# Kernel optimization log

Measured on AMD Instinct MI355X. Metric: run time of the kernel, lower is better.

Reference implementation:

```python
import jax, jax.numpy as jnp
import numpy as np

D_MODEL = 1024
N_HEADS = 16
D_HEAD = 64
N_CTX = 2048
ROTARY_DIM = 64
ROTARY_BASE = 10000.0
ATTN_SCALE = 8.0
IGNORE = -100000.0


def _sin_cos(seq_len):
    # rotary_adjacent_pairs=False -> freq repeated as '(2 d)'
    pos = jnp.arange(seq_len, dtype=jnp.float32)
    dim = jnp.arange(ROTARY_DIM // 2, dtype=jnp.float32)
    freq = ROTARY_BASE ** (dim / (ROTARY_DIM / 2))
    freq = jnp.concatenate([freq, freq])  # (2 d)
    angles = pos[:, None] / freq[None, :]  # [S, rotary_dim]
    return jnp.sin(angles), jnp.cos(angles)


def _apply_rotary(x, sin, cos):
    # x: [B, S, H, d_head]; rotary_dim == d_head here, pass-through part is empty
    x_rot = x[..., :ROTARY_DIM]
    x_pass = x[..., ROTARY_DIM:]
    n = ROTARY_DIM // 2
    x_flip = jnp.concatenate([-x_rot[..., n:], x_rot[..., :n]], axis=-1)
    x_rotated = x_rot * cos[None, :, None, :] + x_flip * sin[None, :, None, :]
    return jnp.concatenate([x_rotated, x_pass], axis=-1)


def setup_inputs() -> dict:
    key = jax.random.key(0)
    ks = jax.random.split(key, 12)
    B, S = 1, 2048
    f = lambda k, shp, s=1.0: jax.random.normal(k, shp, dtype=jnp.float32) * s
    return {
        "xq": f(ks[0], (B, S, N_HEADS, D_MODEL)),
        "xk": f(ks[1], (B, S, N_HEADS, D_MODEL)),
        "xv": f(ks[2], (B, S, N_HEADS, D_MODEL)),
        "W_Q": f(ks[3], (N_HEADS, D_MODEL, D_HEAD), 0.02),
        "b_Q": jnp.zeros((N_HEADS, D_HEAD), jnp.float32),
        "W_K": f(ks[4], (N_HEADS, D_MODEL, D_HEAD), 0.02),
        "b_K": jnp.zeros((N_HEADS, D_HEAD), jnp.float32),
        "W_V": f(ks[5], (N_HEADS, D_MODEL, D_HEAD), 0.02),
        "b_V": jnp.zeros((N_HEADS, D_HEAD), jnp.float32),
        "W_O": f(ks[6], (N_HEADS, D_HEAD, D_MODEL), 0.02),
        "b_O": jnp.zeros((D_MODEL,), jnp.float32),
    }


def reference(xq, xk, xv, W_Q, b_Q, W_K, b_K, W_V, b_V, W_O, b_O):
    S = xq.shape[1]
    sin, cos = _sin_cos(S)
    # per-head QKV projections: [B,S,H,dm] x [H,dm,dh] -> [B,S,H,dh]
    q = jnp.einsum('bsnd,nde->bsne', xq, W_Q) + b_Q
    k = jnp.einsum('bsnd,nde->bsne', xk, W_K) + b_K
    v = jnp.einsum('bsnd,nde->bsne', xv, W_V) + b_V
    q = _apply_rotary(q, sin, cos)
    k = _apply_rotary(k, sin, cos)
    # attention scores [B,H,Q,K]
    scores = jnp.einsum('bqne,bkne->bnqk', q, k) / ATTN_SCALE
    causal = jnp.triu(jnp.ones((S, S), dtype=bool), k=1)
    scores = jnp.where(causal[None, None], IGNORE, scores)
    pattern = jax.nn.softmax(scores, axis=-1)
    z = jnp.einsum('bnqk,bkne->bqne', pattern, v)
    # NOTE: faithful to source — head dim is NOT summed; b_O divided by n_heads
    attn_out = jnp.einsum('bqne,ned->bqnd', z, W_O) + b_O / N_HEADS
    return attn_out
```

## Files before the change

### kernel.cpp

```cpp
#include <hip/hip_runtime.h>
#include <hip/hip_bf16.h>
#include <stdint.h>
#include <math.h>

typedef __bf16 bf16_t;
typedef __bf16 bf16x8 __attribute__((ext_vector_type(8)));
typedef __bf16 bf16x4 __attribute__((ext_vector_type(4)));
typedef float  f32x4  __attribute__((ext_vector_type(4)));

#define S_CTX 2048
#define NH    16
#define DM    1024
#define DH    64

#define WS_WT   0
#define WS_WOT  (3*1048576)
#define WS_Q    (4*1048576)
#define WS_K    (WS_Q  + 2097152)
#define WS_VT   (WS_K  + 2097152)
#define WS_Z    (WS_VT + 2097152)

__device__ __forceinline__ void stage_tile(const bf16_t* __restrict__ g, int row_stride,
                                           bf16_t* lds, int tid) {
#pragma unroll
  for (int i = 0; i < 2; i++) {
    int r = (tid >> 3) + i * 32;
    int c = (tid & 7) << 3;
    *reinterpret_cast<uint4*>(lds + r * 64 + c) =
        *reinterpret_cast<const uint4*>(g + r * row_stride + c);
  }
}

__device__ __forceinline__ void stage_f32(const float* __restrict__ g, int row_stride,
                                          bf16_t* lds, int tid) {
#pragma unroll
  for (int i = 0; i < 4; i++) {
    int idx = tid + i * 256;
    int r = idx >> 4;
    int c = (idx & 15) << 2;
    float4 v = *reinterpret_cast<const float4*>(g + r * row_stride + c);
    bf16x4 b;
    b[0] = (bf16_t)v.x; b[1] = (bf16_t)v.y; b[2] = (bf16_t)v.z; b[3] = (bf16_t)v.w;
    *reinterpret_cast<bf16x4*>(lds + r * 64 + c) = b;
  }
}

__global__ __launch_bounds__(256) void transpose_w(const float* __restrict__ wq,
                                                   const float* __restrict__ wk,
                                                   const float* __restrict__ wv,
                                                   const float* __restrict__ wo,
                                                   bf16_t* __restrict__ ws) {
  __shared__ bf16_t tl[64 * 68];
  int m = blockIdx.z, h = blockIdx.y, t = blockIdx.x, tid = threadIdx.x;
  const float* in; bf16_t* out; int R, C, r0, c0;
  if (m < 3) { in = (m == 0) ? wq : (m == 1) ? wk : wv; out = ws + m * 1048576;
               R = 1024; C = 64; r0 = t * 64; c0 = 0; }
  else       { in = wo; out = ws + WS_WOT; R = 64; C = 1024; r0 = 0; c0 = t * 64; }
  in  += h * 65536;
  out += h * 65536;
#pragma unroll
  for (int i = 0; i < 4; i++) {
    int idx = tid + i * 256;
    int r = idx >> 4, c = (idx & 15) << 2;
    float4 v = *reinterpret_cast<const float4*>(in + (r0 + r) * C + c0 + c);
    bf16x4 b;
    b[0] = (bf16_t)v.x; b[1] = (bf16_t)v.y; b[2] = (bf16_t)v.z; b[3] = (bf16_t)v.w;
    *reinterpret_cast<bf16x4*>(tl + r * 68 + c) = b;
  }
  __syncthreads();
#pragma unroll
  for (int i = 0; i < 2; i++) {
    int oc = (tid >> 3) + i * 32, ok = (tid & 7) << 3;
    bf16x8 v;
#pragma unroll
    for (int j = 0; j < 8; j++) v[j] = tl[(ok + j) * 68 + oc];
    *reinterpret_cast<bf16x8*>(out + (c0 + oc) * R + r0 + ok) = v;
  }
}

__global__ __launch_bounds__(256) void qkv_proj(const float* __restrict__ xq,
                                                const float* __restrict__ xk,
                                                const float* __restrict__ xv,
                                                const float* __restrict__ bq,
                                                const float* __restrict__ bk,
                                                const float* __restrict__ bv,
                                                bf16_t* __restrict__ ws) {
  __shared__ bf16_t Al[64 * 64];
  __shared__ bf16_t Bl[64 * 64];
  int st = blockIdx.x, h = blockIdx.y, m = blockIdx.z;
  int tid = threadIdx.x, w = tid >> 6, lane = tid & 63, quad = lane >> 4, l15 = lane & 15;
  const float*  in   = (m == 0) ? xq : (m == 1) ? xk : xv;
  const bf16_t* wT   = ws + m * 1048576 + h * 65536;
  const float*  bias = (m == 0) ? bq : (m == 1) ? bk : bv;
  int s0 = st * 64;
  f32x4 acc[4];
#pragma unroll
  for (int t = 0; t < 4; t++) acc[t] = (f32x4){0.f, 0.f, 0.f, 0.f};
  const float* Ab = in + (s0 * 16 + h) * 1024;

  for (int k0 = 0; k0 < 1024; k0 += 64) {
    stage_f32(Ab + k0, 16384, Al, tid);
    stage_tile(wT + k0, 1024, Bl, tid);
    __syncthreads();
#pragma unroll
    for (int ks = 0; ks < 2; ks++) {
      bf16x8 af = *reinterpret_cast<const bf16x8*>(Al + (w * 16 + l15) * 64 + ks * 32 + quad * 8);
#pragma unroll
      for (int t = 0; t < 4; t++) {
        bf16x8 bfr = *reinterpret_cast<const bf16x8*>(Bl + (t * 16 + l15) * 64 + ks * 32 + quad * 8);
        acc[t] = __builtin_amdgcn_mfma_f32_16x16x32_bf16(af, bfr, acc[t], 0, 0, 0);
      }
    }
    __syncthreads();
  }
#pragma unroll
  for (int t = 0; t < 4; t++) {
    float bval = bias[h * 64 + t * 16 + l15];
#pragma unroll
    for (int r = 0; r < 4; r++) acc[t][r] += bval;
  }

  if (m < 2) {
    bf16_t* outp = ws + ((m == 0) ? WS_Q : WS_K) + h * (2048 * 64);
#pragma unroll
    for (int t = 0; t < 2; t++) {
      int c_lo = t * 16 + l15;
      float freq = powf(10000.0f, (float)c_lo * (1.0f / 32.0f));
#pragma unroll
      for (int r = 0; r < 4; r++) {
        int s = s0 + w * 16 + quad * 4 + r;
        float ang = (float)s / freq;
        float sv = sinf(ang), cv = cosf(ang);
        float xl = acc[t][r], xh = acc[t + 2][r];
        acc[t][r]     = xl * cv - xh * sv;
        acc[t + 2][r] = xh * cv + xl * sv;
      }
    }
#pragma unroll
    for (int t = 0; t < 4; t++)
#pragma unroll
      for (int r = 0; r < 4; r++) {
        int s = s0 + w * 16 + quad * 4 + r;
        outp[s * 64 + t * 16 + l15] = (bf16_t)acc[t][r];
      }
  } else {
    bf16_t* outp = ws + WS_VT + h * (64 * 2048);
#pragma unroll
    for (int t = 0; t < 4; t++) {
      int e = t * 16 + l15;
      int s = s0 + w * 16 + quad * 4;
      bf16x4 v;
#pragma unroll
      for (int r = 0; r < 4; r++) v[r] = (bf16_t)acc[t][r];
      *reinterpret_cast<bf16x4*>(outp + e * 2048 + s) = v;
    }
  }
}

__global__ __launch_bounds__(256) void attn(bf16_t* __restrict__ ws) {
  __shared__ bf16_t Ql[64 * 64], Kl[64 * 64], Vl[64 * 64], Pl[4 * 16 * 64];
  int qt = blockIdx.x, h = blockIdx.y;
  int tid = threadIdx.x, w = tid >> 6, lane = tid & 63, quad = lane >> 4, l15 = lane & 15;
  const bf16_t* qp  = ws + WS_Q  + h * 131072;
  const bf16_t* kp  = ws + WS_K  + h * 131072;
  const bf16_t* vtp = ws + WS_VT + h * 131072;
  bf16_t*       zp  = ws + WS_Z  + h * 131072;
  int s0 = qt * 64;

  stage_tile(qp + s0 * 64, 64, Ql, tid);

  f32x4 o[4];
#pragma unroll
  for (int t = 0; t < 4; t++) o[t] = (f32x4){0.f, 0.f, 0.f, 0.f};
  float m_i[4], l_i[4];
#pragma unroll
  for (int r = 0; r < 4; r++) { m_i[r] = -__builtin_inff(); l_i[r] = 0.f; }

  for (int j = 0; j <= qt; j++) {
    __syncthreads();
    stage_tile(kp + j * 64 * 64, 64,   Kl, tid);
    stage_tile(vtp + j * 64,     2048, Vl, tid);
    __syncthreads();

    f32x4 sc[4];
#pragma unroll
    for (int t = 0; t < 4; t++) sc[t] = (f32x4){0.f, 0.f, 0.f, 0.f};
#pragma unroll
    for (int ks = 0; ks < 2; ks++) {
      bf16x8 af = *reinterpret_cast<const bf16x8*>(Ql + (w * 16 + l15) * 64 + ks * 32 + quad * 8);
#pragma unroll
      for (int t = 0; t < 4; t++) {
        bf16x8 bfr = *reinterpret_cast<const bf16x8*>(Kl + (t * 16 + l15) * 64 + ks * 32 + quad * 8);
        sc[t] = __builtin_amdgcn_mfma_f32_16x16x32_bf16(af, bfr, sc[t], 0, 0, 0);
      }
    }
#pragma unroll
    for (int t = 0; t < 4; t++) {
      int kvc = j * 64 + t * 16 + l15;
#pragma unroll
      for (int r = 0; r < 4; r++) {
        int qrow = s0 + w * 16 + quad * 4 + r;
        float sv = sc[t][r] * 0.125f;
        sc[t][r] = (kvc > qrow) ? -1e30f : sv;
      }
    }
    float p[4][4], alpha[4];
#pragma unroll
    for (int r = 0; r < 4; r++) {
      float mx = fmaxf(fmaxf(sc[0][r], sc[1][r]), fmaxf(sc[2][r], sc[3][r]));
#pragma unroll
      for (int off = 1; off < 16; off <<= 1) mx = fmaxf(mx, __shfl_xor(mx, off));
      float mn = fmaxf(m_i[r], mx);
      alpha[r] = __expf(m_i[r] - mn);
      float rs = 0.f;
#pragma unroll
      for (int t = 0; t < 4; t++) { p[t][r] = __expf(sc[t][r] - mn); rs += p[t][r]; }
#pragma unroll
      for (int off = 1; off < 16; off <<= 1) rs += __shfl_xor(rs, off);
      l_i[r] = l_i[r] * alpha[r] + rs;
      m_i[r] = mn;
    }
#pragma unroll
    for (int t = 0; t < 4; t++)
#pragma unroll
      for (int r = 0; r < 4; r++)
        Pl[w * 1024 + (quad * 4 + r) * 64 + t * 16 + l15] = (bf16_t)p[t][r];
#pragma unroll
    for (int t = 0; t < 4; t++)
#pragma unroll
      for (int r = 0; r < 4; r++) o[t][r] *= alpha[r];
    __syncthreads();
#pragma unroll
    for (int ks = 0; ks < 2; ks++) {
      bf16x8 af = *reinterpret_cast<const bf16x8*>(Pl + w * 1024 + l15 * 64 + ks * 32 + quad * 8);
#pragma unroll
      for (int t = 0; t < 4; t++) {
        bf16x8 bfr = *reinterpret_cast<const bf16x8*>(Vl + (t * 16 + l15) * 64 + ks * 32 + quad * 8);
        o[t] = __builtin_amdgcn_mfma_f32_16x16x32_bf16(af, bfr, o[t], 0, 0, 0);
      }
    }
  }
  float inv[4];
#pragma unroll
  for (int r = 0; r < 4; r++) inv[r] = 1.0f / l_i[r];
#pragma unroll
  for (int t = 0; t < 4; t++)
#pragma unroll
    for (int r = 0; r < 4; r++) {
      int s = s0 + w * 16 + quad * 4 + r;
      zp[s * 64 + t * 16 + l15] = (bf16_t)(o[t][r] * inv[r]);
    }
}

__global__ __launch_bounds__(256) void out_proj(const bf16_t* __restrict__ ws,
                                                const float* __restrict__ bo,
                                                float* __restrict__ out) {
  __shared__ bf16_t Al[64 * 64], Bl[64 * 64];
  int st = blockIdx.x >> 4, dt = blockIdx.x & 15, h = blockIdx.y;
  int tid = threadIdx.x, w = tid >> 6, lane = tid & 63, quad = lane >> 4, l15 = lane & 15;
  int s0 = st * 64, d0 = dt * 64;
  const bf16_t* zp = ws + WS_Z + h * 131072 + s0 * 64;
  const bf16_t* wo = ws + WS_WOT + h * 65536 + d0 * 64;
  stage_tile(zp, 64, Al, tid);
  stage_tile(wo, 64, Bl, tid);
  __syncthreads();
  f32x4 acc[4];
#pragma unroll
  for (int t = 0; t < 4; t++) acc[t] = (f32x4){0.f, 0.f, 0.f, 0.f};
#pragma unroll
  for (int ks = 0; ks < 2; ks++) {
    bf16x8 af = *reinterpret_cast<const bf16x8*>(Al + (w * 16 + l15) * 64 + ks * 32 + quad * 8);
#pragma unroll
    for (int t = 0; t < 4; t++) {
      bf16x8 bfr = *reinterpret_cast<const bf16x8*>(Bl + (t * 16 + l15) * 64 + ks * 32 + quad * 8);
      acc[t] = __builtin_amdgcn_mfma_f32_16x16x32_bf16(af, bfr, acc[t], 0, 0, 0);
    }
  }
#pragma unroll
  for (int t = 0; t < 4; t++) {
    float bval = bo[d0 + t * 16 + l15] * (1.0f / 16.0f);
#pragma unroll
    for (int r = 0; r < 4; r++) {
      int s = s0 + w * 16 + quad * 4 + r;
      out[(s * 16 + h) * 1024 + d0 + t * 16 + l15] = acc[t][r] + bval;
    }
  }
}

extern "C" void kernel_launch(void* const* d_in, const int* in_sizes, int n_in,
                              void* d_out, int out_size, void* d_ws, size_t ws_size,
                              hipStream_t stream) {
  const float* xq = (const float*)d_in[0];
  const float* xk = (const float*)d_in[1];
  const float* xv = (const float*)d_in[2];
  const float* wq = (const float*)d_in[3];
  const float* bq = (const float*)d_in[4];
  const float* wk = (const float*)d_in[5];
  const float* bk = (const float*)d_in[6];
  const float* wv = (const float*)d_in[7];
  const float* bv = (const float*)d_in[8];
  const float* wo = (const float*)d_in[9];
  const float* bo = (const float*)d_in[10];
  bf16_t* ws  = (bf16_t*)d_ws;
  float*  out = (float*)d_out;

  hipLaunchKernelGGL(transpose_w, dim3(16, 16, 4), dim3(256), 0, stream, wq, wk, wv, wo, ws);
  hipLaunchKernelGGL(qkv_proj,    dim3(32, 16, 3), dim3(256), 0, stream, xq, xk, xv, bq, bk, bv, ws);
  hipLaunchKernelGGL(attn,        dim3(32, 16),    dim3(256), 0, stream, ws);
  hipLaunchKernelGGL(out_proj,    dim3(512, 16),   dim3(256), 0, stream, ws, bo, out);
}
```

Baseline: 570.7 us.

## Enlarge tiles in projection and attention kernels and pad LDS rows

The QKV projection now computes 128 rows per block with a K step of 128, so each B fragment feeds two MFMAs and each block issues more global loads per barrier. The attention kernel processes 128-key tiles per iteration, halving the loop trip count. It also drops the block barrier before the P·V product, since each wave only reads its own P slice. The output projection uses 128x128 tiles, and all LDS tiles get padded row strides (72/136) to reduce bank conflicts. The cost is more LDS and registers per block, fewer blocks in flight, and some fully masked key columns on the last attention tile.

Result: faster. 556.6 us (-2.5%).

```diff
diff --git a/kernel.cpp b/kernel.cpp
--- a/kernel.cpp
+++ b/kernel.cpp
@@ -19,31 +19,6 @@
 #define WS_K    (WS_Q  + 2097152)
 #define WS_VT   (WS_K  + 2097152)
 #define WS_Z    (WS_VT + 2097152)
-
-__device__ __forceinline__ void stage_tile(const bf16_t* __restrict__ g, int row_stride,
-                                           bf16_t* lds, int tid) {
-#pragma unroll
-  for (int i = 0; i < 2; i++) {
-    int r = (tid >> 3) + i * 32;
-    int c = (tid & 7) << 3;
-    *reinterpret_cast<uint4*>(lds + r * 64 + c) =
-        *reinterpret_cast<const uint4*>(g + r * row_stride + c);
-  }
-}
-
-__device__ __forceinline__ void stage_f32(const float* __restrict__ g, int row_stride,
-                                          bf16_t* lds, int tid) {
-#pragma unroll
-  for (int i = 0; i < 4; i++) {
-    int idx = tid + i * 256;
-    int r = idx >> 4;
-    int c = (idx & 15) << 2;
-    float4 v = *reinterpret_cast<const float4*>(g + r * row_stride + c);
-    bf16x4 b;
-    b[0] = (bf16_t)v.x; b[1] = (bf16_t)v.y; b[2] = (bf16_t)v.z; b[3] = (bf16_t)v.w;
-    *reinterpret_cast<bf16x4*>(lds + r * 64 + c) = b;
-  }
-}
 
 __global__ __launch_bounds__(256) void transpose_w(const float* __restrict__ wq,
                                                    const float* __restrict__ wk,
@@ -85,30 +60,52 @@
                                                 const float* __restrict__ bk,
                                                 const float* __restrict__ bv,
                                                 bf16_t* __restrict__ ws) {
-  __shared__ bf16_t Al[64 * 64];
-  __shared__ bf16_t Bl[64 * 64];
+  __shared__ bf16_t Al[128 * 136];
+  __shared__ bf16_t Bl[64 * 136];
   int st = blockIdx.x, h = blockIdx.y, m = blockIdx.z;
   int tid = threadIdx.x, w = tid >> 6, lane = tid & 63, quad = lane >> 4, l15 = lane & 15;
   const float*  in   = (m == 0) ? xq : (m == 1) ? xk : xv;
   const bf16_t* wT   = ws + m * 1048576 + h * 65536;
   const float*  bias = (m == 0) ? bq : (m == 1) ? bk : bv;
-  int s0 = st * 64;
-  f32x4 acc[4];
-#pragma unroll
-  for (int t = 0; t < 4; t++) acc[t] = (f32x4){0.f, 0.f, 0.f, 0.f};
+  int s0 = st * 128;
   const float* Ab = in + (s0 * 16 + h) * 1024;
 
-  for (int k0 = 0; k0 < 1024; k0 += 64) {
-    stage_f32(Ab + k0, 16384, Al, tid);
-    stage_tile(wT + k0, 1024, Bl, tid);
+  f32x4 acc[2][4];
+#pragma unroll
+  for (int rt = 0; rt < 2; rt++)
+#pragma unroll
+    for (int t = 0; t < 4; t++) acc[rt][t] = (f32x4){0.f, 0.f, 0.f, 0.f};
+
+  for (int k0 = 0; k0 < 1024; k0 += 128) {
+#pragma unroll
+    for (int i = 0; i < 8; i++) {
+      int g = tid + i * 256;
+      int r = g >> 4, cg = g & 15;
+      const float* p = Ab + r * 16384 + k0 + cg * 8;
+      float4 v0 = *reinterpret_cast<const float4*>(p);
+      float4 v1 = *reinterpret_cast<const float4*>(p + 4);
+      bf16x8 b;
+      b[0] = (bf16_t)v0.x; b[1] = (bf16_t)v0.y; b[2] = (bf16_t)v0.z; b[3] = (bf16_t)v0.w;
+      b[4] = (bf16_t)v1.x; b[5] = (bf16_t)v1.y; b[6] = (bf16_t)v1.z; b[7] = (bf16_t)v1.w;
+      *reinterpret_cast<bf16x8*>(Al + r * 136 + cg * 8) = b;
+    }
+#pragma unroll
+    for (int i = 0; i < 4; i++) {
+      int g = tid + i * 256;
+      int r = g >> 4, cg = g & 15;
+      *reinterpret_cast<uint4*>(Bl + r * 136 + cg * 8) =
+          *reinterpret_cast<const uint4*>(wT + r * 1024 + k0 + cg * 8);
+    }
     __syncthreads();
 #pragma unroll
-    for (int ks = 0; ks < 2; ks++) {
-      bf16x8 af = *reinterpret_cast<const bf16x8*>(Al + (w * 16 + l15) * 64 + ks * 32 + quad * 8);
+    for (int ks = 0; ks < 4; ks++) {
+      bf16x8 a0 = *reinterpret_cast<const bf16x8*>(Al + (w * 32 + l15) * 136 + ks * 32 + quad * 8);
+      bf16x8 a1 = *reinterpret_cast<const bf16x8*>(Al + (w * 32 + 16 + l15) * 136 + ks * 32 + quad * 8);
 #pragma unroll
       for (int t = 0; t < 4; t++) {
-        bf16x8 bfr = *reinterpret_cast<const bf16x8*>(Bl + (t * 16 + l15) * 64 + ks * 32 + quad * 8);
-        acc[t] = __builtin_amdgcn_mfma_f32_16x16x32_bf16(af, bfr, acc[t], 0, 0, 0);
+        bf16x8 bb = *reinterpret_cast<const bf16x8*>(Bl + (t * 16 + l15) * 136 + ks * 32 + quad * 8);
+        acc[0][t] = __builtin_amdgcn_mfma_f32_16x16x32_bf16(a0, bb, acc[0][t], 0, 0, 0);
+        acc[1][t] = __builtin_amdgcn_mfma_f32_16x16x32_bf16(a1, bb, acc[1][t], 0, 0, 0);
       }
     }
     __syncthreads();
@@ -117,7 +114,9 @@
   for (int t = 0; t < 4; t++) {
     float bval = bias[h * 64 + t * 16 + l15];
 #pragma unroll
-    for (int r = 0; r < 4; r++) acc[t][r] += bval;
+    for (int rt = 0; rt < 2; rt++)
+#pragma unroll
+      for (int r = 0; r < 4; r++) acc[rt][t][r] += bval;
   }
 
   if (m < 2) {
@@ -127,38 +126,47 @@
       int c_lo = t * 16 + l15;
       float freq = powf(10000.0f, (float)c_lo * (1.0f / 32.0f));
 #pragma unroll
-      for (int r = 0; r < 4; r++) {
-        int s = s0 + w * 16 + quad * 4 + r;
-        float ang = (float)s / freq;
-        float sv = sinf(ang), cv = cosf(ang);
-        float xl = acc[t][r], xh = acc[t + 2][r];
-        acc[t][r]     = xl * cv - xh * sv;
-        acc[t + 2][r] = xh * cv + xl * sv;
-      }
-    }
-#pragma unroll
-    for (int t = 0; t < 4; t++)
-#pragma unroll
-      for (int r = 0; r < 4; r++) {
-        int s = s0 + w * 16 + quad * 4 + r;
-        outp[s * 64 + t * 16 + l15] = (bf16_t)acc[t][r];
-      }
+      for (int rt = 0; rt < 2; rt++)
+#pragma unroll
+        for (int r = 0; r < 4; r++) {
+          int s = s0 + w * 32 + rt * 16 + quad * 4 + r;
+          float ang = (float)s / freq;
+          float sv = sinf(ang), cv = cosf(ang);
+          float xl = acc[rt][t][r], xh = acc[rt][t + 2][r];
+          acc[rt][t][r]     = xl * cv - xh * sv;
+          acc[rt][t + 2][r] = xh * cv + xl * sv;
+        }
+    }
+#pragma unroll
+    for (int rt = 0; rt < 2; rt++)
+#pragma unroll
+      for (int t = 0; t < 4; t++)
+#pragma unroll
+        for (int r = 0; r < 4; r++) {
+          int s = s0 + w * 32 + rt * 16 + quad * 4 + r;
+          outp[s * 64 + t * 16 + l15] = (bf16_t)acc[rt][t][r];
+        }
   } else {
     bf16_t* outp = ws + WS_VT + h * (64 * 2048);
 #pragma unroll
-    for (int t = 0; t < 4; t++) {
-      int e = t * 16 + l15;
-      int s = s0 + w * 16 + quad * 4;
-      bf16x4 v;
-#pragma unroll
-      for (int r = 0; r < 4; r++) v[r] = (bf16_t)acc[t][r];
-      *reinterpret_cast<bf16x4*>(outp + e * 2048 + s) = v;
-    }
+    for (int rt = 0; rt < 2; rt++)
+#pragma unroll
+      for (int t = 0; t < 4; t++) {
+        int e = t * 16 + l15;
+        int sbase = s0 + w * 32 + rt * 16 + quad * 4;
+        bf16x4 v;
+#pragma unroll
+        for (int r = 0; r < 4; r++) v[r] = (bf16_t)acc[rt][t][r];
+        *reinterpret_cast<bf16x4*>(outp + e * 2048 + sbase) = v;
+      }
   }
 }
 
 __global__ __launch_bounds__(256) void attn(bf16_t* __restrict__ ws) {
-  __shared__ bf16_t Ql[64 * 64], Kl[64 * 64], Vl[64 * 64], Pl[4 * 16 * 64];
+  __shared__ bf16_t Ql[64 * 72];
+  __shared__ bf16_t Kl[128 * 72];
+  __shared__ bf16_t Vl[64 * 136];
+  __shared__ bf16_t Pl[4 * 16 * 136];
   int qt = blockIdx.x, h = blockIdx.y;
   int tid = threadIdx.x, w = tid >> 6, lane = tid & 63, quad = lane >> 4, l15 = lane & 15;
   const bf16_t* qp  = ws + WS_Q  + h * 131072;
@@ -167,7 +175,13 @@
   bf16_t*       zp  = ws + WS_Z  + h * 131072;
   int s0 = qt * 64;
 
-  stage_tile(qp + s0 * 64, 64, Ql, tid);
+#pragma unroll
+  for (int i = 0; i < 2; i++) {
+    int g = tid + i * 256;
+    int r = g >> 3, cg = g & 7;
+    *reinterpret_cast<uint4*>(Ql + r * 72 + cg * 8) =
+        *reinterpret_cast<const uint4*>(qp + (s0 + r) * 64 + cg * 8);
+  }
 
   f32x4 o[4];
 #pragma unroll
@@ -175,28 +189,42 @@
   float m_i[4], l_i[4];
 #pragma unroll
   for (int r = 0; r < 4; r++) { m_i[r] = -__builtin_inff(); l_i[r] = 0.f; }
-
-  for (int j = 0; j <= qt; j++) {
+  bf16_t* Plw = Pl + w * (16 * 136);
+
+  int jmax = qt >> 1;
+  for (int j = 0; j <= jmax; j++) {
     __syncthreads();
-    stage_tile(kp + j * 64 * 64, 64,   Kl, tid);
-    stage_tile(vtp + j * 64,     2048, Vl, tid);
+#pragma unroll
+    for (int i = 0; i < 4; i++) {
+      int g = tid + i * 256;
+      int r = g >> 3, cg = g & 7;
+      *reinterpret_cast<uint4*>(Kl + r * 72 + cg * 8) =
+          *reinterpret_cast<const uint4*>(kp + (j * 128 + r) * 64 + cg * 8);
+    }
+#pragma unroll
+    for (int i = 0; i < 4; i++) {
+      int g = tid + i * 256;
+      int r = g >> 4, cg = g & 15;
+      *reinterpret_cast<uint4*>(Vl + r * 136 + cg * 8) =
+          *reinterpret_cast<const uint4*>(vtp + r * 2048 + j * 128 + cg * 8);
+    }
     __syncthreads();
 
-    f32x4 sc[4];
-#pragma unroll
-    for (int t = 0; t < 4; t++) sc[t] = (f32x4){0.f, 0.f, 0.f, 0.f};
+    f32x4 sc[8];
+#pragma unroll
+    for (int t = 0; t < 8; t++) sc[t] = (f32x4){0.f, 0.f, 0.f, 0.f};
 #pragma unroll
     for (int ks = 0; ks < 2; ks++) {
-      bf16x8 af = *reinterpret_cast<const bf16x8*>(Ql + (w * 16 + l15) * 64 + ks * 32 + quad * 8);
-#pragma unroll
-      for (int t = 0; t < 4; t++) {
-        bf16x8 bfr = *reinterpret_cast<const bf16x8*>(Kl + (t * 16 + l15) * 64 + ks * 32 + quad * 8);
+      bf16x8 af = *reinterpret_cast<const bf16x8*>(Ql + (w * 16 + l15) * 72 + ks * 32 + quad * 8);
+#pragma unroll
+      for (int t = 0; t < 8; t++) {
+        bf16x8 bfr = *reinterpret_cast<const bf16x8*>(Kl + (t * 16 + l15) * 72 + ks * 32 + quad * 8);
         sc[t] = __builtin_amdgcn_mfma_f32_16x16x32_bf16(af, bfr, sc[t], 0, 0, 0);
       }
     }
 #pragma unroll
-    for (int t = 0; t < 4; t++) {
-      int kvc = j * 64 + t * 16 + l15;
+    for (int t = 0; t < 8; t++) {
+      int kvc = j * 128 + t * 16 + l15;
 #pragma unroll
       for (int r = 0; r < 4; r++) {
         int qrow = s0 + w * 16 + quad * 4 + r;
@@ -204,38 +232,39 @@
         sc[t][r] = (kvc > qrow) ? -1e30f : sv;
       }
     }
-    float p[4][4], alpha[4];
+    float alpha[4];
 #pragma unroll
     for (int r = 0; r < 4; r++) {
-      float mx = fmaxf(fmaxf(sc[0][r], sc[1][r]), fmaxf(sc[2][r], sc[3][r]));
+      float mx = sc[0][r];
+#pragma unroll
+      for (int t = 1; t < 8; t++) mx = fmaxf(mx, sc[t][r]);
 #pragma unroll
       for (int off = 1; off < 16; off <<= 1) mx = fmaxf(mx, __shfl_xor(mx, off));
       float mn = fmaxf(m_i[r], mx);
       alpha[r] = __expf(m_i[r] - mn);
       float rs = 0.f;
 #pragma unroll
-      for (int t = 0; t < 4; t++) { p[t][r] = __expf(sc[t][r] - mn); rs += p[t][r]; }
+      for (int t = 0; t < 8; t++) { sc[t][r] = __expf(sc[t][r] - mn); rs += sc[t][r]; }
 #pragma unroll
       for (int off = 1; off < 16; off <<= 1) rs += __shfl_xor(rs, off);
       l_i[r] = l_i[r] * alpha[r] + rs;
       m_i[r] = mn;
     }
 #pragma unroll
+    for (int t = 0; t < 8; t++)
+#pragma unroll
+      for (int r = 0; r < 4; r++)
+        Plw[(quad * 4 + r) * 136 + t * 16 + l15] = (bf16_t)sc[t][r];
+#pragma unroll
     for (int t = 0; t < 4; t++)
 #pragma unroll
-      for (int r = 0; r < 4; r++)
-        Pl[w * 1024 + (quad * 4 + r) * 64 + t * 16 + l15] = (bf16_t)p[t][r];
-#pragma unroll
-    for (int t = 0; t < 4; t++)
-#pragma unroll
       for (int r = 0; r < 4; r++) o[t][r] *= alpha[r];
-    __syncthreads();
-#pragma unroll
-    for (int ks = 0; ks < 2; ks++) {
-      bf16x8 af = *reinterpret_cast<const bf16x8*>(Pl + w * 1024 + l15 * 64 + ks * 32 + quad * 8);
+#pragma unroll
+    for (int ks = 0; ks < 4; ks++) {
+      bf16x8 af = *reinterpret_cast<const bf16x8*>(Plw + l15 * 136 + ks * 32 + quad * 8);
 #pragma unroll
       for (int t = 0; t < 4; t++) {
-        bf16x8 bfr = *reinterpret_cast<const bf16x8*>(Vl + (t * 16 + l15) * 64 + ks * 32 + quad * 8);
+        bf16x8 bfr = *reinterpret_cast<const bf16x8*>(Vl + (t * 16 + l15) * 136 + ks * 32 + quad * 8);
         o[t] = __builtin_amdgcn_mfma_f32_16x16x32_bf16(af, bfr, o[t], 0, 0, 0);
       }
     }
@@ -255,35 +284,54 @@
 __global__ __launch_bounds__(256) void out_proj(const bf16_t* __restrict__ ws,
                                                 const float* __restrict__ bo,
                                                 float* __restrict__ out) {
-  __shared__ bf16_t Al[64 * 64], Bl[64 * 64];
-  int st = blockIdx.x >> 4, dt = blockIdx.x & 15, h = blockIdx.y;
+  __shared__ bf16_t Zl[128 * 72];
+  __shared__ bf16_t Wl[128 * 72];
+  int st = blockIdx.x >> 3, dt = blockIdx.x & 7, h = blockIdx.y;
   int tid = threadIdx.x, w = tid >> 6, lane = tid & 63, quad = lane >> 4, l15 = lane & 15;
-  int s0 = st * 64, d0 = dt * 64;
-  const bf16_t* zp = ws + WS_Z + h * 131072 + s0 * 64;
-  const bf16_t* wo = ws + WS_WOT + h * 65536 + d0 * 64;
-  stage_tile(zp, 64, Al, tid);
-  stage_tile(wo, 64, Bl, tid);
+  int s0 = st * 128, d0 = dt * 128;
+  const bf16_t* zp = ws + WS_Z + h * 131072;
+  const bf16_t* wo = ws + WS_WOT + h * 65536;
+#pragma unroll
+  for (int i = 0; i < 4; i++) {
+    int g = tid + i * 256;
+    int r = g >> 3, cg = g & 7;
+    *reinterpret_cast<uint4*>(Zl + r * 72 + cg * 8) =
+        *reinterpret_cast<const uint4*>(zp + (s0 + r) * 64 + cg * 8);
+  }
+#pragma unroll
+  for (int i = 0; i < 4; i++) {
+    int g = tid + i * 256;
+    int r = g >> 3, cg = g & 7;
+    *reinterpret_cast<uint4*>(Wl + r * 72 + cg * 8) =
+        *reinterpret_cast<const uint4*>(wo + (d0 + r) * 64 + cg * 8);
+  }
   __syncthreads();
-  f32x4 acc[4];
-#pragma unroll
-  for (int t = 0; t < 4; t++) acc[t] = (f32x4){0.f, 0.f, 0.f, 0.f};
+  f32x4 acc[2][8];
+#pragma unroll
+  for (int rt = 0; rt < 2; rt++)
+#pragma unroll
+    for (int t = 0; t < 8; t++) acc[rt][t] = (f32x4){0.f, 0.f, 0.f, 0.f};
 #pragma unroll
   for (int ks = 0; ks < 2; ks++) {
-    bf16x8 af = *reinterpret_cast<const bf16x8*>(Al + (w * 16 + l15) * 64 + ks * 32 + quad * 8);
-#pragma unroll
-    for (int t = 0; t < 4; t++) {
-      bf16x8 bfr = *reinterpret_cast<const bf16x8*>(Bl + (t * 16 + l15) * 64 + ks * 32 + quad * 8);
-      acc[t] = __builtin_amdgcn_mfma_f32_16x16x32_bf16(af, bfr, acc[t], 0, 0, 0);
-    }
-  }
-#pragma unroll
-  for (int t = 0; t < 4; t++) {
+    bf16x8 a0 = *reinterpret_cast<const bf16x8*>(Zl + (w * 32 + l15) * 72 + ks * 32 + quad * 8);
+    bf16x8 a1 = *reinterpret_cast<const bf16x8*>(Zl + (w * 32 + 16 + l15) * 72 + ks * 32 + quad * 8);
+#pragma unroll
+    for (int t = 0; t < 8; t++) {
+      bf16x8 bb = *reinterpret_cast<const bf16x8*>(Wl + (t * 16 + l15) * 72 + ks * 32 + quad * 8);
+      acc[0][t] = __builtin_amdgcn_mfma_f32_16x16x32_bf16(a0, bb, acc[0][t], 0, 0, 0);
+      acc[1][t] = __builtin_amdgcn_mfma_f32_16x16x32_bf16(a1, bb, acc[1][t], 0, 0, 0);
+    }
+  }
+#pragma unroll
+  for (int t = 0; t < 8; t++) {
     float bval = bo[d0 + t * 16 + l15] * (1.0f / 16.0f);
 #pragma unroll
-    for (int r = 0; r < 4; r++) {
-      int s = s0 + w * 16 + quad * 4 + r;
-      out[(s * 16 + h) * 1024 + d0 + t * 16 + l15] = acc[t][r] + bval;
-    }
+    for (int rt = 0; rt < 2; rt++)
+#pragma unroll
+      for (int r = 0; r < 4; r++) {
+        int s = s0 + w * 32 + rt * 16 + quad * 4 + r;
+        out[(s * 16 + h) * 1024 + d0 + t * 16 + l15] = acc[rt][t][r] + bval;
+      }
   }
 }
 
@@ -305,7 +353,7 @@
   float*  out = (float*)d_out;
 
   hipLaunchKernelGGL(transpose_w, dim3(16, 16, 4), dim3(256), 0, stream, wq, wk, wv, wo, ws);
-  hipLaunchKernelGGL(qkv_proj,    dim3(32, 16, 3), dim3(256), 0, stream, xq, xk, xv, bq, bk, bv, ws);
+  hipLaunchKernelGGL(qkv_proj,    dim3(16, 16, 3), dim3(256), 0, stream, xq, xk, xv, bq, bk, bv, ws);
   hipLaunchKernelGGL(attn,        dim3(32, 16),    dim3(256), 0, stream, ws);
-  hipLaunchKernelGGL(out_proj,    dim3(512, 16),   dim3(256), 0, stream, ws, bo, out);
-}
+  hipLaunchKernelGGL(out_proj,    dim3(128, 16),   dim3(256), 0, stream, ws, bo, out);
+}
```
